# Performance work log

Measured on AMD Instinct MI355X. Metric: run time of the kernel, lower is better.

## Reference

```python
import jax, jax.numpy as jnp
import numpy as np


def _gat_layer(h, mask, w, a_src, a_dst):
    # h: [B,C,N,Fin], w: [C,H,Fin,Fout], a_*: [C,H,Fout,1], mask: [B,N,N] (True where no edge)
    h_prime = jnp.einsum('bcni,chio->bchno', h, w)          # [B,C,H,N,Fout]
    t = jnp.tanh(h_prime)
    s = jnp.einsum('bchno,cho->bchn', t, a_src[..., 0])      # src scores
    d = jnp.einsum('bchno,cho->bchn', t, a_dst[..., 0])      # dst scores
    attn = s[..., :, None] + d[..., None, :]                 # [B,C,H,N,N]
    attn = jnp.where(attn >= 0, attn, 0.2 * attn)            # leaky_relu(0.2)
    attn = jnp.where(mask[:, None, None, :, :], jnp.float32(-1e12), attn)
    attn = jax.nn.softmax(attn, axis=-1)
    return jnp.einsum('bchnm,bchmo->bchno', attn, h_prime)   # [B,C,H,N,Fout]


def setup_inputs() -> dict:
    key = jax.random.key(0)
    ks = jax.random.split(key, 8)
    B, C, N, F0, H, F = 2, 2, 1024, 64, 8, 64

    def xavier(k, shape):
        fan_in, fan_out = shape[-2], shape[-1]
        lim = (6.0 / (fan_in + fan_out)) ** 0.5
        return jax.random.uniform(k, shape, jnp.float32, -lim, lim)

    x = jax.random.normal(ks[0], (B, C, N, F0), dtype=jnp.float32)
    adj = jax.random.randint(ks[1], (B, N, N), 0, 2, dtype=jnp.int32)
    w1 = xavier(ks[2], (C, H, F0, F))
    a_src1 = xavier(ks[3], (C, H, F, 1))
    a_dst1 = xavier(ks[4], (C, H, F, 1))
    w2 = xavier(ks[5], (C, H, H * F, F))
    a_src2 = xavier(ks[6], (C, H, F, 1))
    a_dst2 = xavier(ks[7], (C, H, F, 1))
    return {"x": x, "adj": adj, "w1": w1, "a_src1": a_src1, "a_dst1": a_dst1,
            "w2": w2, "a_src2": a_src2, "a_dst2": a_dst2}


def reference(x, adj, w1, a_src1, a_dst1, w2, a_src2, a_dst2):
    B, C, N, _ = x.shape
    adj_f = adj.astype(jnp.float32) + jnp.eye(N, dtype=jnp.float32)[None]  # add self-loops
    mask = adj_f == 0                                        # [B,N,N]
    out1 = _gat_layer(x, mask, w1, a_src1, a_dst1)           # [B,C,H,N,F]
    # permute heads next to features, flatten, elu (dropout is identity in eval)
    x1 = jax.nn.elu(jnp.transpose(out1, (0, 1, 3, 2, 4)).reshape(B, C, N, -1))
    out2 = _gat_layer(x1, mask, w2, a_src2, a_dst2)          # [B,C,H,N,F]
    return out2.mean(axis=2)                                 # mean over heads -> [B,C,N,F]
```

## Files before the change

kernel.cpp:

```cpp
#include <hip/hip_runtime.h>
#include <hip/hip_bf16.h>

#define BB 2
#define CC 2
#define NN 1024
#define HH 8
#define FFV 64
#define BCHN (BB*CC*HH)
#define SVN  (BB*CC*HH*NN)

typedef _Float16 f16x8 __attribute__((ext_vector_type(8)));
typedef _Float16 f16x4 __attribute__((ext_vector_type(4)));
typedef __fp16 h16x2 __attribute__((ext_vector_type(2)));
typedef float f32x4 __attribute__((ext_vector_type(4)));

__global__ __launch_bounds__(256) void prep_kernel(
    const int* __restrict__ adj, const float* __restrict__ w1, const float* __restrict__ w2,
    _Float16* __restrict__ w1T, _Float16* __restrict__ w2T,
    unsigned long long* __restrict__ bmg)
{
  __shared__ __align__(16) _Float16 tile[64*72];
  const int bx = blockIdx.x;
  const int t = threadIdx.x;
  if (bx < 144) {
    int ch, k0, K; const float* w; _Float16* wT;
    if (bx < 16) { ch = bx; k0 = 0; K = 64; w = w1; wT = w1T; }
    else { const int u = bx - 16; ch = u >> 3; k0 = (u & 7)*64; K = 512; w = w2; wT = w2T; }
    const float* src = w + ((size_t)ch*K + k0)*64;
    #pragma unroll
    for (int j = 0; j < 4; ++j) {
      const int u = t + j*256;
      const int k = u >> 4, seg = u & 15;
      const float4 v = ((const float4*)src)[(size_t)k*16 + seg];
      tile[(seg*4+0)*72 + k] = (_Float16)v.x;
      tile[(seg*4+1)*72 + k] = (_Float16)v.y;
      tile[(seg*4+2)*72 + k] = (_Float16)v.z;
      tile[(seg*4+3)*72 + k] = (_Float16)v.w;
    }
    __syncthreads();
    _Float16* dst = wT + (size_t)ch*64*K + k0;
    #pragma unroll
    for (int j = 0; j < 2; ++j) {
      const int u = t + j*256;
      const int f = u >> 3, seg = u & 7;
      const f16x8 o = *(const f16x8*)&tile[f*72 + seg*8];
      *(f16x8*)(dst + (size_t)f*K + seg*8) = o;
    }
  } else {
    const int wg = (bx - 144)*4 + (t >> 6);
    const int lane = t & 63;
    for (int idx = wg; idx < BB*NN*16; idx += 1024) {
      const int b = idx >> 14;
      const int n = (idx >> 4) & (NN - 1);
      const int word = idx & 15;
      const int m = word*64 + lane;
      const int pred = (adj[((size_t)b*NN + n)*NN + m] != 0) || (m == n);
      unsigned long long bits = __ballot(pred);
      if (lane == 0) bmg[idx] = bits;
    }
  }
}

__global__ __launch_bounds__(256) void proj1_mfma(
    const float* __restrict__ x,
    const _Float16* __restrict__ wT,
    const float* __restrict__ asrc, const float* __restrict__ adst,
    _Float16* __restrict__ HpT, float* __restrict__ s_out, float* __restrict__ d_out)
{
  __shared__ float sp[4][32], sd[4][32];
  const int bch = blockIdx.y;
  const int h = bch % HH; const int bc = bch / HH; const int c = bc % CC;
  const int row0 = blockIdx.x*32;
  const int t = threadIdx.x;
  const int w = t >> 6, lane = t & 63;
  const int colr = lane & 15, quad = lane >> 4;

  const float* Ar0 = x + ((size_t)bc*NN + row0 + colr)*64;
  const float* Ar1 = Ar0 + (size_t)16*64;
  const _Float16* Brow = wT + ((size_t)(c*HH + h)*64 + w*16 + colr)*64;

  f32x4 acc0 = {0.f,0.f,0.f,0.f}, acc1 = {0.f,0.f,0.f,0.f};
  #pragma unroll
  for (int kb = 0; kb < 64; kb += 32) {
    const float4 u0 = *(const float4*)(Ar0 + kb + quad*8);
    const float4 u1 = *(const float4*)(Ar0 + kb + quad*8 + 4);
    const float4 v0 = *(const float4*)(Ar1 + kb + quad*8);
    const float4 v1 = *(const float4*)(Ar1 + kb + quad*8 + 4);
    union { f16x8 v; h16x2 h[4]; } a0, a1;
    a0.h[0] = __builtin_amdgcn_cvt_pkrtz(u0.x, u0.y);
    a0.h[1] = __builtin_amdgcn_cvt_pkrtz(u0.z, u0.w);
    a0.h[2] = __builtin_amdgcn_cvt_pkrtz(u1.x, u1.y);
    a0.h[3] = __builtin_amdgcn_cvt_pkrtz(u1.z, u1.w);
    a1.h[0] = __builtin_amdgcn_cvt_pkrtz(v0.x, v0.y);
    a1.h[1] = __builtin_amdgcn_cvt_pkrtz(v0.z, v0.w);
    a1.h[2] = __builtin_amdgcn_cvt_pkrtz(v1.x, v1.y);
    a1.h[3] = __builtin_amdgcn_cvt_pkrtz(v1.z, v1.w);
    const f16x8 bf = *(const f16x8*)(Brow + kb + quad*8);
    acc0 = __builtin_amdgcn_mfma_f32_16x16x32_f16(a0.v, bf, acc0, 0, 0, 0);
    acc1 = __builtin_amdgcn_mfma_f32_16x16x32_f16(a1.v, bf, acc1, 0, 0, 0);
  }

  const float af = asrc[(c*HH + h)*64 + w*16 + colr];
  const float bf_ = adst[(c*HH + h)*64 + w*16 + colr];
  _Float16* HT = HpT + ((size_t)bch*64 + w*16 + colr)*NN + row0;

  #pragma unroll
  for (int mt = 0; mt < 2; ++mt) {
    const f32x4 a = mt ? acc1 : acc0;
    f16x4 hv;
    #pragma unroll
    for (int i = 0; i < 4; ++i) {
      const float v = a[i];
      hv[i] = (_Float16)v;
      const float ex = __expf(2.f*v);
      const float th = 1.f - 2.f/(ex + 1.f);
      float ps = th * af, pd = th * bf_;
      #pragma unroll
      for (int off = 1; off < 16; off <<= 1) {
        ps += __shfl_xor(ps, off);
        pd += __shfl_xor(pd, off);
      }
      if (colr == 0) {
        sp[w][mt*16 + quad*4 + i] = ps;
        sd[w][mt*16 + quad*4 + i] = pd;
      }
    }
    *(f16x4*)(HT + mt*16 + quad*4) = hv;
  }
  __syncthreads();
  if (t < 32) {
    const float sv = sp[0][t] + sp[1][t] + sp[2][t] + sp[3][t];
    const float dv = sd[0][t] + sd[1][t] + sd[2][t] + sd[3][t];
    s_out[bch*NN + row0 + t] = sv;
    d_out[bch*NN + row0 + t] = dv;
  }
}

__global__ __launch_bounds__(256) void proj2_mfma(
    const _Float16* __restrict__ A,
    const _Float16* __restrict__ wT,
    const float* __restrict__ asrc, const float* __restrict__ adst,
    _Float16* __restrict__ HpT, float* __restrict__ s_out, float* __restrict__ d_out)
{
  const int K = 512;
  __shared__ float sp[4][32], sd[4][32];
  const int bch = blockIdx.y;
  const int h = bch % HH; const int bc = bch / HH; const int c = bc % CC;
  const int row0 = blockIdx.x*32;
  const int t = threadIdx.x;
  const int w = t >> 6, lane = t & 63;
  const int colr = lane & 15, quad = lane >> 4;

  const _Float16* Arow0 = A + ((size_t)bc*NN + row0 + colr)*K;
  const _Float16* Arow1 = Arow0 + (size_t)16*K;
  const _Float16* Brow  = wT + ((size_t)(c*HH + h)*64 + w*16 + colr)*K;

  f32x4 acc0 = {0.f,0.f,0.f,0.f}, acc1 = {0.f,0.f,0.f,0.f};
  #pragma unroll 4
  for (int kb = 0; kb < K; kb += 32) {
    const f16x8 a0 = *(const f16x8*)(Arow0 + kb + quad*8);
    const f16x8 a1 = *(const f16x8*)(Arow1 + kb + quad*8);
    const f16x8 bf = *(const f16x8*)(Brow  + kb + quad*8);
    acc0 = __builtin_amdgcn_mfma_f32_16x16x32_f16(a0, bf, acc0, 0, 0, 0);
    acc1 = __builtin_amdgcn_mfma_f32_16x16x32_f16(a1, bf, acc1, 0, 0, 0);
  }

  const float af = asrc[(c*HH + h)*64 + w*16 + colr];
  const float bf_ = adst[(c*HH + h)*64 + w*16 + colr];
  _Float16* HT = HpT + ((size_t)bch*64 + w*16 + colr)*NN + row0;

  #pragma unroll
  for (int mt = 0; mt < 2; ++mt) {
    const f32x4 a = mt ? acc1 : acc0;
    f16x4 hv;
    #pragma unroll
    for (int i = 0; i < 4; ++i) {
      const float v = a[i];
      hv[i] = (_Float16)v;
      const float ex = __expf(2.f*v);
      const float th = 1.f - 2.f/(ex + 1.f);
      float ps = th * af, pd = th * bf_;
      #pragma unroll
      for (int off = 1; off < 16; off <<= 1) {
        ps += __shfl_xor(ps, off);
        pd += __shfl_xor(pd, off);
      }
      if (colr == 0) {
        sp[w][mt*16 + quad*4 + i] = ps;
        sd[w][mt*16 + quad*4 + i] = pd;
      }
    }
    *(f16x4*)(HT + mt*16 + quad*4) = hv;
  }
  __syncthreads();
  if (t < 32) {
    const float sv = sp[0][t] + sp[1][t] + sp[2][t] + sp[3][t];
    const float dv = sd[0][t] + sd[1][t] + sd[2][t] + sd[3][t];
    s_out[bch*NN + row0 + t] = sv;
    d_out[bch*NN + row0 + t] = dv;
  }
}

template<int LAYER>
__global__ __launch_bounds__(256, 4) void attn_mfma(
    const _Float16* __restrict__ HpT, const float* __restrict__ s_arr,
    const float* __restrict__ d_arr, const unsigned long long* __restrict__ bmg,
    _Float16* __restrict__ outp)
{
  __shared__ float partials[4][32*68];
  __shared__ float dsP[4][32];
  const int bch = blockIdx.x;
  const int b = bch / (CC*HH);
  const int row0 = blockIdx.y*32;
  const int t = threadIdx.x;
  const int w = t >> 6, lane = t & 63;
  const int colr = lane & 15, quad = lane >> 4;

  const float* dg = d_arr + (size_t)bch*NN;
  const float4* dg4 = (const float4*)dg;
  float mxl = -1e30f;
  #pragma unroll
  for (int j = 0; j < 4; ++j) {
    const float4 v = dg4[lane + 64*j];
    mxl = fmaxf(fmaxf(v.x, v.y), fmaxf(fmaxf(v.z, v.w), mxl));
  }
  #pragma unroll
  for (int off = 1; off < 64; off <<= 1) mxl = fmaxf(mxl, __shfl_xor(mxl, off));
  const float maxd = mxl;

  const int r0 = row0 + colr, r1 = r0 + 16;
  const float s0 = s_arr[(size_t)bch*NN + r0];
  const float s1 = s_arr[(size_t)bch*NN + r1];
  const float so0 = s0 + maxd, so1 = s1 + maxd;
  const float offs0 = fmaxf(so0, 0.2f*so0);
  const float offs1 = fmaxf(so1, 0.2f*so1);
  const float sA0 = s0 - offs0, sB0 = 0.2f*s0 - offs0;
  const float sA1 = s1 - offs1, sB1 = 0.2f*s1 - offs1;

  unsigned long long m0[4], m1[4];
  {
    const unsigned long long* bm0 = bmg + ((size_t)b*NN + r0)*16 + w*4;
    const unsigned long long* bm1 = bmg + ((size_t)b*NN + r1)*16 + w*4;
    #pragma unroll
    for (int j = 0; j < 4; ++j) { m0[j] = bm0[j]; m1[j] = bm1[j]; }
  }

  const _Float16* Bg = HpT + (size_t)bch*64*NN;
  const int kbase = w*256;
  const _Float16* Bp = Bg + kbase + quad*8;

  f32x4 acc[2][4], accs[2];
  #pragma unroll
  for (int rt = 0; rt < 2; ++rt) {
    accs[rt] = (f32x4){0.f,0.f,0.f,0.f};
    #pragma unroll
    for (int ft = 0; ft < 4; ++ft) acc[rt][ft] = (f32x4){0.f,0.f,0.f,0.f};
  }
  f16x8 ones;
  #pragma unroll
  for (int i = 0; i < 8; ++i) ones[i] = (_Float16)1.f;

  f16x8 Bb[3][4];
  float4 db[3][2];
  #pragma unroll
  for (int j = 0; j < 2; ++j) {
    #pragma unroll
    for (int ft = 0; ft < 4; ++ft)
      Bb[j][ft] = *(const f16x8*)(Bp + (size_t)(ft*16 + colr)*NN + j*32);
    db[j][0] = *(const float4*)(dg + kbase + j*32 + quad*8);
    db[j][1] = *(const float4*)(dg + kbase + j*32 + quad*8 + 4);
  }

  #pragma unroll
  for (int ks = 0; ks < 8; ++ks) {
    const int cur = ks % 3;
    if (ks < 6) {
      const int nxt = (ks + 2) % 3;
      #pragma unroll
      for (int ft = 0; ft < 4; ++ft)
        Bb[nxt][ft] = *(const f16x8*)(Bp + (size_t)(ft*16 + colr)*NN + (ks+2)*32);
      db[nxt][0] = *(const float4*)(dg + kbase + (ks+2)*32 + quad*8);
      db[nxt][1] = *(const float4*)(dg + kbase + (ks+2)*32 + quad*8 + 4);
    }
    const unsigned mb0 = (unsigned)((m0[ks >> 1] >> ((ks & 1)*32 + quad*8)) & 0xFFull);
    const unsigned mb1 = (unsigned)((m1[ks >> 1] >> ((ks & 1)*32 + quad*8)) & 0xFFull);
    const float4 dc0 = db[cur][0], dc1 = db[cur][1];
    const float dd[8] = {dc0.x, dc0.y, dc0.z, dc0.w, dc1.x, dc1.y, dc1.z, dc1.w};
    union { f16x8 v; h16x2 h[4]; } A0, A1;
    #pragma unroll
    for (int jp = 0; jp < 4; ++jp) {
      float p0[2], p1[2];
      #pragma unroll
      for (int jj = 0; jj < 2; ++jj) {
        const int j = jp*2 + jj;
        const float dj = dd[j];
        const float l0 = fmaxf(sA0 + dj, fmaf(0.2f, dj, sB0));
        const float l1 = fmaxf(sA1 + dj, fmaf(0.2f, dj, sB1));
        p0[jj] = ((mb0 >> j) & 1u) ? __expf(l0) : 0.f;
        p1[jj] = ((mb1 >> j) & 1u) ? __expf(l1) : 0.f;
      }
      A0.h[jp] = __builtin_amdgcn_cvt_pkrtz(p0[0], p0[1]);
      A1.h[jp] = __builtin_amdgcn_cvt_pkrtz(p1[0], p1[1]);
    }
    #pragma unroll
    for (int ft = 0; ft < 4; ++ft) {
      acc[0][ft] = __builtin_amdgcn_mfma_f32_16x16x32_f16(A0.v, Bb[cur][ft], acc[0][ft], 0, 0, 0);
      acc[1][ft] = __builtin_amdgcn_mfma_f32_16x16x32_f16(A1.v, Bb[cur][ft], acc[1][ft], 0, 0, 0);
    }
    accs[0] = __builtin_amdgcn_mfma_f32_16x16x32_f16(A0.v, ones, accs[0], 0, 0, 0);
    accs[1] = __builtin_amdgcn_mfma_f32_16x16x32_f16(A1.v, ones, accs[1], 0, 0, 0);
  }

  if (colr == 0) {
    #pragma unroll
    for (int i = 0; i < 4; ++i) {
      dsP[w][quad*4 + i] = accs[0][i];
      dsP[w][16 + quad*4 + i] = accs[1][i];
    }
  }
  float* pw = partials[w];
  #pragma unroll
  for (int rt = 0; rt < 2; ++rt)
    #pragma unroll
    for (int ft = 0; ft < 4; ++ft)
      #pragma unroll
      for (int i = 0; i < 4; ++i)
        pw[(rt*16 + quad*4 + i)*68 + ft*16 + colr] = acc[rt][ft][i];
  __syncthreads();

  const int r = t >> 3, f0 = (t & 7)*8;
  const float dsum = dsP[0][r] + dsP[1][r] + dsP[2][r] + dsP[3][r];
  const float inv = 1.f / dsum;
  float4 c0 = {0.f,0.f,0.f,0.f}, c1 = {0.f,0.f,0.f,0.f};
  #pragma unroll
  for (int w4 = 0; w4 < 4; ++w4) {
    const float* base = &partials[w4][r*68 + f0];
    const float4 a0 = *(const float4*)base;
    const float4 a1 = *(const float4*)(base + 4);
    c0.x += a0.x; c0.y += a0.y; c0.z += a0.z; c0.w += a0.w;
    c1.x += a1.x; c1.y += a1.y; c1.z += a1.z; c1.w += a1.w;
  }
  const float cv[8] = {c0.x,c0.y,c0.z,c0.w, c1.x,c1.y,c1.z,c1.w};
  f16x8 o;
  #pragma unroll
  for (int i = 0; i < 8; ++i) {
    float v = cv[i] * inv;
    if (LAYER == 1) v = v > 0.f ? v : expm1f(v);
    o[i] = (_Float16)v;
  }
  const int bc = bch / HH, h = bch % HH;
  if (LAYER == 1)
    *(f16x8*)(outp + ((size_t)bc*NN + row0 + r)*512 + h*64 + f0) = o;
  else
    *(f16x8*)(outp + ((size_t)bch*NN + row0 + r)*64 + f0) = o;
}

__global__ __launch_bounds__(256) void reduce_heads(
    const _Float16* __restrict__ out2, float* __restrict__ out)
{
  const int o = blockIdx.x*256 + threadIdx.x;
  const int f = o & 63;
  const int n = (o >> 6) & (NN - 1);
  const int bc = o >> 16;
  float acc = 0.f;
  #pragma unroll
  for (int h = 0; h < HH; ++h)
    acc += (float)out2[(((size_t)bc*HH + h)*NN + n)*FFV + f];
  out[o] = acc * 0.125f;
}

extern "C" void kernel_launch(void* const* d_in, const int* in_sizes, int n_in,
                              void* d_out, int out_size, void* d_ws, size_t ws_size,
                              hipStream_t stream)
{
  const float* x   = (const float*)d_in[0];
  const int*   adj = (const int*)d_in[1];
  const float* w1  = (const float*)d_in[2];
  const float* as1 = (const float*)d_in[3];
  const float* ad1 = (const float*)d_in[4];
  const float* w2  = (const float*)d_in[5];
  const float* as2 = (const float*)d_in[6];
  const float* ad2 = (const float*)d_in[7];

  char* w8 = (char*)d_ws;
  _Float16* HpT = (_Float16*)(w8);
  _Float16* XB  = (_Float16*)(w8 + (4u<<20));
  _Float16* w1T = (_Float16*)(w8 + (8u<<20));
  _Float16* w2T = (_Float16*)(w8 + (8u<<20) + (256u<<10));
  float* s_v = (float*)(w8 + (10u<<20));
  float* d_v = (float*)(w8 + (10u<<20) + SVN*4);
  unsigned long long* bmg = (unsigned long long*)(w8 + (10u<<20) + SVN*8);

  prep_kernel<<<400, 256, 0, stream>>>(adj, w1, w2, w1T, w2T, bmg);
  proj1_mfma<<<dim3(NN/32, BCHN), 256, 0, stream>>>(x, w1T, as1, ad1, HpT, s_v, d_v);
  attn_mfma<1><<<dim3(BCHN, NN/32), 256, 0, stream>>>(HpT, s_v, d_v, bmg, XB);
  proj2_mfma<<<dim3(NN/32, BCHN), 256, 0, stream>>>(XB, w2T, as2, ad2, HpT, s_v, d_v);
  attn_mfma<2><<<dim3(BCHN, NN/32), 256, 0, stream>>>(HpT, s_v, d_v, bmg, XB);
  reduce_heads<<<dim3(1024), 256, 0, stream>>>(XB, (float*)d_out);
}
```

Baseline: 167.7 us.

## Halve attention row tile to 16 and drop register prefetch for higher occupancy

The attention kernel now gives each block 16 query rows instead of 32, which doubles the grid. The 3-deep register prefetch of B and d tiles is replaced by direct loads on each step, and launch bounds go from 4 to 8 blocks per SM to raise occupancy and hide latency. The cost is that every B tile load from HpT now feeds half as many rows, so global/L2 traffic for the values doubles. The d-max reduction is also repeated in twice as many blocks, and the loads lose the explicit latency hiding they had before.

```diff
diff --git a/kernel.cpp b/kernel.cpp
--- a/kernel.cpp
+++ b/kernel.cpp
@@ -202,16 +202,16 @@
 }
 
 template<int LAYER>
-__global__ __launch_bounds__(256, 4) void attn_mfma(
+__global__ __launch_bounds__(256, 8) void attn_mfma(
     const _Float16* __restrict__ HpT, const float* __restrict__ s_arr,
     const float* __restrict__ d_arr, const unsigned long long* __restrict__ bmg,
     _Float16* __restrict__ outp)
 {
-  __shared__ float partials[4][32*68];
-  __shared__ float dsP[4][32];
+  __shared__ float partials[4][16*68];
+  __shared__ float dsP[4][16];
   const int bch = blockIdx.x;
   const int b = bch / (CC*HH);
-  const int row0 = blockIdx.y*32;
+  const int row0 = blockIdx.y*16;
   const int t = threadIdx.x;
   const int w = t >> 6, lane = t & 63;
   const int colr = lane & 15, quad = lane >> 4;
@@ -228,131 +228,94 @@
   for (int off = 1; off < 64; off <<= 1) mxl = fmaxf(mxl, __shfl_xor(mxl, off));
   const float maxd = mxl;
 
-  const int r0 = row0 + colr, r1 = r0 + 16;
+  const int r0 = row0 + colr;
   const float s0 = s_arr[(size_t)bch*NN + r0];
-  const float s1 = s_arr[(size_t)bch*NN + r1];
-  const float so0 = s0 + maxd, so1 = s1 + maxd;
+  const float so0 = s0 + maxd;
   const float offs0 = fmaxf(so0, 0.2f*so0);
-  const float offs1 = fmaxf(so1, 0.2f*so1);
   const float sA0 = s0 - offs0, sB0 = 0.2f*s0 - offs0;
-  const float sA1 = s1 - offs1, sB1 = 0.2f*s1 - offs1;
-
-  unsigned long long m0[4], m1[4];
+
+  unsigned long long m0[4];
   {
     const unsigned long long* bm0 = bmg + ((size_t)b*NN + r0)*16 + w*4;
-    const unsigned long long* bm1 = bmg + ((size_t)b*NN + r1)*16 + w*4;
-    #pragma unroll
-    for (int j = 0; j < 4; ++j) { m0[j] = bm0[j]; m1[j] = bm1[j]; }
+    #pragma unroll
+    for (int j = 0; j < 4; ++j) m0[j] = bm0[j];
   }
 
   const _Float16* Bg = HpT + (size_t)bch*64*NN;
   const int kbase = w*256;
   const _Float16* Bp = Bg + kbase + quad*8;
 
-  f32x4 acc[2][4], accs[2];
-  #pragma unroll
-  for (int rt = 0; rt < 2; ++rt) {
-    accs[rt] = (f32x4){0.f,0.f,0.f,0.f};
-    #pragma unroll
-    for (int ft = 0; ft < 4; ++ft) acc[rt][ft] = (f32x4){0.f,0.f,0.f,0.f};
-  }
+  f32x4 acc[4], accs;
+  accs = (f32x4){0.f,0.f,0.f,0.f};
+  #pragma unroll
+  for (int ft = 0; ft < 4; ++ft) acc[ft] = (f32x4){0.f,0.f,0.f,0.f};
   f16x8 ones;
   #pragma unroll
   for (int i = 0; i < 8; ++i) ones[i] = (_Float16)1.f;
 
-  f16x8 Bb[3][4];
-  float4 db[3][2];
-  #pragma unroll
-  for (int j = 0; j < 2; ++j) {
+  #pragma unroll
+  for (int ks = 0; ks < 8; ++ks) {
+    f16x8 Bc[4];
     #pragma unroll
     for (int ft = 0; ft < 4; ++ft)
-      Bb[j][ft] = *(const f16x8*)(Bp + (size_t)(ft*16 + colr)*NN + j*32);
-    db[j][0] = *(const float4*)(dg + kbase + j*32 + quad*8);
-    db[j][1] = *(const float4*)(dg + kbase + j*32 + quad*8 + 4);
-  }
-
-  #pragma unroll
-  for (int ks = 0; ks < 8; ++ks) {
-    const int cur = ks % 3;
-    if (ks < 6) {
-      const int nxt = (ks + 2) % 3;
-      #pragma unroll
-      for (int ft = 0; ft < 4; ++ft)
-        Bb[nxt][ft] = *(const f16x8*)(Bp + (size_t)(ft*16 + colr)*NN + (ks+2)*32);
-      db[nxt][0] = *(const float4*)(dg + kbase + (ks+2)*32 + quad*8);
-      db[nxt][1] = *(const float4*)(dg + kbase + (ks+2)*32 + quad*8 + 4);
-    }
+      Bc[ft] = *(const f16x8*)(Bp + (size_t)(ft*16 + colr)*NN + ks*32);
+    const float4 dc0 = *(const float4*)(dg + kbase + ks*32 + quad*8);
+    const float4 dc1 = *(const float4*)(dg + kbase + ks*32 + quad*8 + 4);
     const unsigned mb0 = (unsigned)((m0[ks >> 1] >> ((ks & 1)*32 + quad*8)) & 0xFFull);
-    const unsigned mb1 = (unsigned)((m1[ks >> 1] >> ((ks & 1)*32 + quad*8)) & 0xFFull);
-    const float4 dc0 = db[cur][0], dc1 = db[cur][1];
     const float dd[8] = {dc0.x, dc0.y, dc0.z, dc0.w, dc1.x, dc1.y, dc1.z, dc1.w};
-    union { f16x8 v; h16x2 h[4]; } A0, A1;
+    union { f16x8 v; h16x2 h[4]; } A0;
     #pragma unroll
     for (int jp = 0; jp < 4; ++jp) {
-      float p0[2], p1[2];
+      float p0[2];
       #pragma unroll
       for (int jj = 0; jj < 2; ++jj) {
         const int j = jp*2 + jj;
         const float dj = dd[j];
         const float l0 = fmaxf(sA0 + dj, fmaf(0.2f, dj, sB0));
-        const float l1 = fmaxf(sA1 + dj, fmaf(0.2f, dj, sB1));
         p0[jj] = ((mb0 >> j) & 1u) ? __expf(l0) : 0.f;
-        p1[jj] = ((mb1 >> j) & 1u) ? __expf(l1) : 0.f;
       }
       A0.h[jp] = __builtin_amdgcn_cvt_pkrtz(p0[0], p0[1]);
-      A1.h[jp] = __builtin_amdgcn_cvt_pkrtz(p1[0], p1[1]);
-    }
-    #pragma unroll
-    for (int ft = 0; ft < 4; ++ft) {
-      acc[0][ft] = __builtin_amdgcn_mfma_f32_16x16x32_f16(A0.v, Bb[cur][ft], acc[0][ft], 0, 0, 0);
-      acc[1][ft] = __builtin_amdgcn_mfma_f32_16x16x32_f16(A1.v, Bb[cur][ft], acc[1][ft], 0, 0, 0);
-    }
-    accs[0] = __builtin_amdgcn_mfma_f32_16x16x32_f16(A0.v, ones, accs[0], 0, 0, 0);
-    accs[1] = __builtin_amdgcn_mfma_f32_16x16x32_f16(A1.v, ones, accs[1], 0, 0, 0);
+    }
+    #pragma unroll
+    for (int ft = 0; ft < 4; ++ft)
+      acc[ft] = __builtin_amdgcn_mfma_f32_16x16x32_f16(A0.v, Bc[ft], acc[ft], 0, 0, 0);
+    accs = __builtin_amdgcn_mfma_f32_16x16x32_f16(A0.v, ones, accs, 0, 0, 0);
   }
 
   if (colr == 0) {
     #pragma unroll
-    for (int i = 0; i < 4; ++i) {
-      dsP[w][quad*4 + i] = accs[0][i];
-      dsP[w][16 + quad*4 + i] = accs[1][i];
-    }
+    for (int i = 0; i < 4; ++i) dsP[w][quad*4 + i] = accs[i];
   }
   float* pw = partials[w];
   #pragma unroll
-  for (int rt = 0; rt < 2; ++rt)
-    #pragma unroll
-    for (int ft = 0; ft < 4; ++ft)
-      #pragma unroll
-      for (int i = 0; i < 4; ++i)
-        pw[(rt*16 + quad*4 + i)*68 + ft*16 + colr] = acc[rt][ft][i];
+  for (int ft = 0; ft < 4; ++ft)
+    #pragma unroll
+    for (int i = 0; i < 4; ++i)
+      pw[(quad*4 + i)*68 + ft*16 + colr] = acc[ft][i];
   __syncthreads();
 
-  const int r = t >> 3, f0 = (t & 7)*8;
+  const int r = t >> 4, f0 = (t & 15)*4;
   const float dsum = dsP[0][r] + dsP[1][r] + dsP[2][r] + dsP[3][r];
   const float inv = 1.f / dsum;
-  float4 c0 = {0.f,0.f,0.f,0.f}, c1 = {0.f,0.f,0.f,0.f};
+  float4 c = {0.f,0.f,0.f,0.f};
   #pragma unroll
   for (int w4 = 0; w4 < 4; ++w4) {
-    const float* base = &partials[w4][r*68 + f0];
-    const float4 a0 = *(const float4*)base;
-    const float4 a1 = *(const float4*)(base + 4);
-    c0.x += a0.x; c0.y += a0.y; c0.z += a0.z; c0.w += a0.w;
-    c1.x += a1.x; c1.y += a1.y; c1.z += a1.z; c1.w += a1.w;
-  }
-  const float cv[8] = {c0.x,c0.y,c0.z,c0.w, c1.x,c1.y,c1.z,c1.w};
-  f16x8 o;
-  #pragma unroll
-  for (int i = 0; i < 8; ++i) {
+    const float4 a = *(const float4*)&partials[w4][r*68 + f0];
+    c.x += a.x; c.y += a.y; c.z += a.z; c.w += a.w;
+  }
+  const float cv[4] = {c.x, c.y, c.z, c.w};
+  f16x4 o;
+  #pragma unroll
+  for (int i = 0; i < 4; ++i) {
     float v = cv[i] * inv;
     if (LAYER == 1) v = v > 0.f ? v : expm1f(v);
     o[i] = (_Float16)v;
   }
   const int bc = bch / HH, h = bch % HH;
   if (LAYER == 1)
-    *(f16x8*)(outp + ((size_t)bc*NN + row0 + r)*512 + h*64 + f0) = o;
+    *(f16x4*)(outp + ((size_t)bc*NN + row0 + r)*512 + h*64 + f0) = o;
   else
-    *(f16x8*)(outp + ((size_t)bch*NN + row0 + r)*64 + f0) = o;
+    *(f16x4*)(outp + ((size_t)bch*NN + row0 + r)*64 + f0) = o;
 }
 
 __global__ __launch_bounds__(256) void reduce_heads(
@@ -393,8 +356,8 @@
 
   prep_kernel<<<400, 256, 0, stream>>>(adj, w1, w2, w1T, w2T, bmg);
   proj1_mfma<<<dim3(NN/32, BCHN), 256, 0, stream>>>(x, w1T, as1, ad1, HpT, s_v, d_v);
-  attn_mfma<1><<<dim3(BCHN, NN/32), 256, 0, stream>>>(HpT, s_v, d_v, bmg, XB);
+  attn_mfma<1><<<dim3(BCHN, NN/16), 256, 0, stream>>>(HpT, s_v, d_v, bmg, XB);
   proj2_mfma<<<dim3(NN/32, BCHN), 256, 0, stream>>>(XB, w2T, as2, ad2, HpT, s_v, d_v);
-  attn_mfma<2><<<dim3(BCHN, NN/32), 256, 0, stream>>>(HpT, s_v, d_v, bmg, XB);
+  attn_mfma<2><<<dim3(BCHN, NN/16), 256, 0, stream>>>(HpT, s_v, d_v, bmg, XB);
   reduce_heads<<<dim3(1024), 256, 0, stream>>>(XB, (float*)d_out);
 }
```

New measurement: 200.3 us. +19.4%, slower.
